# Kernel optimization log

Hardware: AMD Instinct MI355X
Metric: run time of the kernel (lower is better)

## Reference

```python
import jax, jax.numpy as jnp
import numpy as np

NEG = -1e30  # acts as -inf for logcumsumexp but keeps grads finite


def setup_inputs() -> dict:
    key = jax.random.key(0)
    k1, k2, k3 = jax.random.split(key, 3)
    B, N, L = 2048, 8192, 512
    y_pred_scores = jax.random.normal(k1, (B, N), dtype=jnp.float32)
    idx = jax.random.randint(k2, (B, L), 0, N)
    # ragged valid lengths in [L//2, L]; positions >= length are padded with -1
    lengths = jax.random.randint(k3, (B, 1), L // 2, L + 1)
    pos = jnp.arange(L)[None, :]
    y_true_seqs = jnp.where(pos < lengths, idx, -1).astype(jnp.int64)
    return {"y_pred_scores": y_pred_scores, "y_true_seqs": y_true_seqs}


def reference(y_pred_scores, y_true_seqs):
    # sanitize (torch_sanitize)
    s = jnp.nan_to_num(y_pred_scores, nan=0.0, posinf=1e6, neginf=-1e6)
    mask = y_true_seqs != -1                      # [B, L]
    idx = jnp.clip(y_true_seqs, 0, s.shape[1] - 1)
    g = jnp.take_along_axis(s, idx, axis=1)       # [B, L] gathered scores
    # Removing padded entries then flip+logcumsumexp+flip == suffix logsumexp
    # over the sequence with padded positions contributing exp(NEG)=0.
    gm = jnp.where(mask, g, NEG)
    log_den = jax.lax.cumlogsumexp(gm[:, ::-1], axis=1)[:, ::-1]  # [B, L]
    ll = jnp.where(mask, g - log_den, 0.0).sum(axis=1)            # [B]
    used = jnp.any(mask, axis=1)                                  # [B]
    total_ll = jnp.where(used, ll, 0.0).sum()
    n_used = used.sum().astype(s.dtype)
    return jnp.where(n_used > 0, -total_ll / n_used, jnp.zeros((), s.dtype))
```

## Files before the change

### kernel.cpp

```cpp
#include <hip/hip_runtime.h>

#define NEGV (-1e30f)
#define IDM  (-1e38f)

struct LSE { float m, s; };

__device__ __forceinline__ LSE lse_comb(LSE a, LSE b) {
    float M = fmaxf(a.m, b.m);
    LSE r;
    r.m = M;
    r.s = a.s * __expf(a.m - M) + b.s * __expf(b.m - M);
    return r;
}

__global__ __launch_bounds__(256) void listnet_row_kernel(
    const float* __restrict__ scores,
    const int*   __restrict__ seqs,
    float2*      __restrict__ part,
    int N, int L)
{
    const int b = blockIdx.x;
    const float* srow = scores + (long long)b * N;
    const int2*  irow = (const int2*)(seqs + (long long)b * L);

    const int t    = threadIdx.x;
    const int lane = t & 63;
    const int wv   = t >> 6;

    int2 ii = irow[t];
    bool v0 = (ii.x != -1), v1 = (ii.y != -1);
    int  c0 = min(max(ii.x, 0), N - 1);
    int  c1 = min(max(ii.y, 0), N - 1);
    float g0 = srow[c0];
    float g1 = srow[c1];
    g0 = isnan(g0) ? 0.f : fminf(fmaxf(g0, -1e6f), 1e6f);
    g1 = isnan(g1) ? 0.f : fminf(fmaxf(g1, -1e6f), 1e6f);
    float x0 = v0 ? g0 : NEGV;
    float x1 = v1 ? g1 : NEGV;

    float M2 = fmaxf(x0, x1);
    LSE inc; inc.m = M2; inc.s = __expf(x0 - M2) + __expf(x1 - M2);

    #pragma unroll
    for (int off = 1; off < 64; off <<= 1) {
        float om = __shfl_down(inc.m, off, 64);
        float os = __shfl_down(inc.s, off, 64);
        if (lane + off < 64) { LSE o; o.m = om; o.s = os; inc = lse_comb(inc, o); }
    }

    __shared__ float wm[4], wsv[4];
    if (lane == 0) { wm[wv] = inc.m; wsv[wv] = inc.s; }

    float em = __shfl_down(inc.m, 1, 64);
    float es = __shfl_down(inc.s, 1, 64);
    LSE exc;
    if (lane < 63) { exc.m = em; exc.s = es; }
    else           { exc.m = IDM; exc.s = 0.f; }

    __syncthreads();

    LSE above; above.m = IDM; above.s = 0.f;
    #pragma unroll
    for (int w2 = 1; w2 < 4; ++w2) {
        if (wv + w2 < 4) { LSE o; o.m = wm[wv + w2]; o.s = wsv[wv + w2]; above = lse_comb(above, o); }
    }
    LSE e_thr = lse_comb(exc, above);

    LSE p1; p1.m = x1; p1.s = 1.f;
    LSE s1 = lse_comb(p1, e_thr);
    float d1 = s1.m + __logf(s1.s);
    LSE p0; p0.m = x0; p0.s = 1.f;
    LSE s0 = lse_comb(p0, s1);
    float d0 = s0.m + __logf(s0.s);

    float ll  = (v1 ? (x1 - d1) : 0.f) + (v0 ? (x0 - d0) : 0.f);
    int   cnt = (int)v0 + (int)v1;

    #pragma unroll
    for (int off = 32; off > 0; off >>= 1) {
        ll  += __shfl_down(ll,  off, 64);
        cnt += __shfl_down(cnt, off, 64);
    }
    __shared__ float lsum[4];
    __shared__ int   csum[4];
    if (lane == 0) { lsum[wv] = ll; csum[wv] = cnt; }
    __syncthreads();
    if (t == 0) {
        float rowll = lsum[0] + lsum[1] + lsum[2] + lsum[3];
        int   rowc  = csum[0] + csum[1] + csum[2] + csum[3];
        float2 r;
        r.x = (rowc > 0) ? rowll : 0.f;
        r.y = (rowc > 0) ? 1.f   : 0.f;
        part[b] = r;
    }
}

__global__ __launch_bounds__(256) void listnet_finalize_kernel(
    const float2* __restrict__ part, float* __restrict__ out, int B)
{
    const int t    = threadIdx.x;
    const int lane = t & 63;
    const int wv   = t >> 6;

    float tot = 0.f, cnt = 0.f;
    for (int i = t; i < B; i += 256) {
        float2 p = part[i];
        tot += p.x;
        cnt += p.y;
    }
    #pragma unroll
    for (int off = 32; off > 0; off >>= 1) {
        tot += __shfl_down(tot, off, 64);
        cnt += __shfl_down(cnt, off, 64);
    }
    __shared__ float ts[4], cs[4];
    if (lane == 0) { ts[wv] = tot; cs[wv] = cnt; }
    __syncthreads();
    if (t == 0) {
        float T = ts[0] + ts[1] + ts[2] + ts[3];
        float C = cs[0] + cs[1] + cs[2] + cs[3];
        out[0] = (C > 0.f) ? (-T / C) : 0.f;
    }
}

extern "C" void kernel_launch(void* const* d_in, const int* in_sizes, int n_in,
                              void* d_out, int out_size, void* d_ws, size_t ws_size,
                              hipStream_t stream) {
    const float* scores = (const float*)d_in[0];
    const int*   seqs   = (const int*)d_in[1];
    float*       out    = (float*)d_out;
    float2*      part   = (float2*)d_ws;

    const int L = 512;
    const int B = in_sizes[1] / L;
    const int N = in_sizes[0] / B;

    listnet_row_kernel<<<B, 256, 0, stream>>>(scores, seqs, part, N, L);
    listnet_finalize_kernel<<<1, 256, 0, stream>>>(part, out, B);
}
```

Baseline: 96.22 us.

## Replace online log-sum-exp scan with global-max plus plain sum scan

The per-row suffix log-sum-exp scan now finds a block-wide max first, then runs a plain additive suffix scan on exp(x - M). This replaces the paired (max, sum) online combine, which cost two shuffles and two exps per step. It adds one extra reduction and barrier and can lose precision when a row's scores span a wide range. The finalize kernel is also shrunk to a single wavefront, and row validity is now taken from the max instead of a count reduction.

```diff
diff --git a/kernel.cpp b/kernel.cpp
--- a/kernel.cpp
+++ b/kernel.cpp
@@ -1,17 +1,6 @@
 #include <hip/hip_runtime.h>
 
 #define NEGV (-1e30f)
-#define IDM  (-1e38f)
-
-struct LSE { float m, s; };
-
-__device__ __forceinline__ LSE lse_comb(LSE a, LSE b) {
-    float M = fmaxf(a.m, b.m);
-    LSE r;
-    r.m = M;
-    r.s = a.s * __expf(a.m - M) + b.s * __expf(b.m - M);
-    return r;
-}
 
 __global__ __launch_bounds__(256) void listnet_row_kernel(
     const float* __restrict__ scores,
@@ -20,8 +9,8 @@
     int N, int L)
 {
     const int b = blockIdx.x;
-    const float* srow = scores + (long long)b * N;
-    const int2*  irow = (const int2*)(seqs + (long long)b * L);
+    const float* srow = scores + (size_t)b * N;
+    const int2*  irow = (const int2*)(seqs + (size_t)b * L);
 
     const int t    = threadIdx.x;
     const int lane = t & 63;
@@ -38,89 +27,72 @@
     float x0 = v0 ? g0 : NEGV;
     float x1 = v1 ? g1 : NEGV;
 
-    float M2 = fmaxf(x0, x1);
-    LSE inc; inc.m = M2; inc.s = __expf(x0 - M2) + __expf(x1 - M2);
+    float mx = fmaxf(x0, x1);
+    #pragma unroll
+    for (int off = 32; off; off >>= 1)
+        mx = fmaxf(mx, __shfl_xor(mx, off, 64));
+    __shared__ float wmax[4];
+    if (lane == 0) wmax[wv] = mx;
+    __syncthreads();
+    const float M = fmaxf(fmaxf(wmax[0], wmax[1]), fmaxf(wmax[2], wmax[3]));
+
+    float e0 = __expf(x0 - M);
+    float e1 = __expf(x1 - M);
+    float S  = e0 + e1;
+    #pragma unroll
+    for (int off = 1; off < 64; off <<= 1) {
+        float o = __shfl_down(S, off, 64);
+        S += (lane + off < 64) ? o : 0.f;
+    }
+    __shared__ float wtot[4];
+    if (lane == 0) wtot[wv] = S;
+    float Safter = __shfl_down(S, 1, 64);
+    if (lane == 63) Safter = 0.f;
+    __syncthreads();
+    float above = 0.f;
+    if (wv < 3) above += wtot[wv + 1];
+    if (wv < 2) above += wtot[wv + 2];
+    if (wv < 1) above += wtot[wv + 3];
+    const float A = Safter + above;
+
+    float s1 = e1 + A;
+    float s0 = e0 + s1;
+    float ll = 0.f;
+    if (v1) ll += x1 - (M + __logf(s1));
+    if (v0) ll += x0 - (M + __logf(s0));
 
     #pragma unroll
-    for (int off = 1; off < 64; off <<= 1) {
-        float om = __shfl_down(inc.m, off, 64);
-        float os = __shfl_down(inc.s, off, 64);
-        if (lane + off < 64) { LSE o; o.m = om; o.s = os; inc = lse_comb(inc, o); }
-    }
-
-    __shared__ float wm[4], wsv[4];
-    if (lane == 0) { wm[wv] = inc.m; wsv[wv] = inc.s; }
-
-    float em = __shfl_down(inc.m, 1, 64);
-    float es = __shfl_down(inc.s, 1, 64);
-    LSE exc;
-    if (lane < 63) { exc.m = em; exc.s = es; }
-    else           { exc.m = IDM; exc.s = 0.f; }
-
-    __syncthreads();
-
-    LSE above; above.m = IDM; above.s = 0.f;
-    #pragma unroll
-    for (int w2 = 1; w2 < 4; ++w2) {
-        if (wv + w2 < 4) { LSE o; o.m = wm[wv + w2]; o.s = wsv[wv + w2]; above = lse_comb(above, o); }
-    }
-    LSE e_thr = lse_comb(exc, above);
-
-    LSE p1; p1.m = x1; p1.s = 1.f;
-    LSE s1 = lse_comb(p1, e_thr);
-    float d1 = s1.m + __logf(s1.s);
-    LSE p0; p0.m = x0; p0.s = 1.f;
-    LSE s0 = lse_comb(p0, s1);
-    float d0 = s0.m + __logf(s0.s);
-
-    float ll  = (v1 ? (x1 - d1) : 0.f) + (v0 ? (x0 - d0) : 0.f);
-    int   cnt = (int)v0 + (int)v1;
-
-    #pragma unroll
-    for (int off = 32; off > 0; off >>= 1) {
-        ll  += __shfl_down(ll,  off, 64);
-        cnt += __shfl_down(cnt, off, 64);
-    }
+    for (int off = 32; off; off >>= 1)
+        ll += __shfl_down(ll, off, 64);
     __shared__ float lsum[4];
-    __shared__ int   csum[4];
-    if (lane == 0) { lsum[wv] = ll; csum[wv] = cnt; }
+    if (lane == 0) lsum[wv] = ll;
     __syncthreads();
     if (t == 0) {
-        float rowll = lsum[0] + lsum[1] + lsum[2] + lsum[3];
-        int   rowc  = csum[0] + csum[1] + csum[2] + csum[3];
+        bool used = (M > -1e29f);
         float2 r;
-        r.x = (rowc > 0) ? rowll : 0.f;
-        r.y = (rowc > 0) ? 1.f   : 0.f;
+        r.x = used ? (lsum[0] + lsum[1] + lsum[2] + lsum[3]) : 0.f;
+        r.y = used ? 1.f : 0.f;
         part[b] = r;
     }
 }
 
-__global__ __launch_bounds__(256) void listnet_finalize_kernel(
+__global__ __launch_bounds__(64) void listnet_finalize_kernel(
     const float2* __restrict__ part, float* __restrict__ out, int B)
 {
-    const int t    = threadIdx.x;
-    const int lane = t & 63;
-    const int wv   = t >> 6;
-
+    const int t = threadIdx.x;
     float tot = 0.f, cnt = 0.f;
-    for (int i = t; i < B; i += 256) {
+    for (int i = t; i < B; i += 64) {
         float2 p = part[i];
         tot += p.x;
         cnt += p.y;
     }
     #pragma unroll
-    for (int off = 32; off > 0; off >>= 1) {
+    for (int off = 32; off; off >>= 1) {
         tot += __shfl_down(tot, off, 64);
         cnt += __shfl_down(cnt, off, 64);
     }
-    __shared__ float ts[4], cs[4];
-    if (lane == 0) { ts[wv] = tot; cs[wv] = cnt; }
-    __syncthreads();
-    if (t == 0) {
-        float T = ts[0] + ts[1] + ts[2] + ts[3];
-        float C = cs[0] + cs[1] + cs[2] + cs[3];
-        out[0] = (C > 0.f) ? (-T / C) : 0.f;
-    }
+    if (t == 0)
+        out[0] = (cnt > 0.f) ? (-tot / cnt) : 0.f;
 }
 
 extern "C" void kernel_launch(void* const* d_in, const int* in_sizes, int n_in,
@@ -136,5 +108,5 @@
     const int N = in_sizes[0] / B;
 
     listnet_row_kernel<<<B, 256, 0, stream>>>(scores, seqs, part, N, L);
-    listnet_finalize_kernel<<<1, 256, 0, stream>>>(part, out, B);
+    listnet_finalize_kernel<<<1, 64, 0, stream>>>(part, out, B);
 }
```

Result: slower. 100.4 us (+4.4%).
